# Optimization experiments

Hardware: AMD Instinct MI355X
Metric: run time of the kernel (lower is better)

The kernel has to match this reference:

```python
import jax
import jax.numpy as jnp
import numpy as np


def setup_inputs() -> dict:
    key = jax.random.key(0)
    k1, k2 = jax.random.split(key)
    B, C, H, W = 2, 256, 64, 128  # 1/8-res RAFT features of a 512x1024 image
    fmap1 = jax.random.normal(k1, (B, C, H, W), dtype=jnp.float32)
    fmap2 = jax.random.normal(k2, (B, C, H, W), dtype=jnp.float32)
    return {"fmap1": fmap1, "fmap2": fmap2, "k": 32}


def reference(fmap1, fmap2, k):
    B, C, H, W = fmap1.shape
    N = H * W
    f1 = fmap1.reshape(B, C, N)
    f2 = fmap2.reshape(B, C, N)

    # --- KNN (FAISS inner-product search), indices are non-differentiable ---
    scores = jnp.einsum('bcn,bcm->bnm', jax.lax.stop_gradient(f1),
                        jax.lax.stop_gradient(f2))  # [B, N1, N2]
    _, idx = jax.lax.top_k(scores, k)               # [B, N1, k]
    idx = jnp.transpose(idx, (0, 2, 1))             # [B, k, N1]

    # --- gather top-k target features: gathered[b,c,j,n] = f2[b,c,idx[b,j,n]] ---
    gathered = jax.vmap(lambda f, i: f[:, i])(f2, idx)  # [B, C, k, N1]

    # --- sparse correlation ---
    corr_sp = jnp.einsum('bcn,bckn->bkn', f1, gathered) / jnp.sqrt(jnp.float32(C))

    # --- coordinate grids (y-first), relative displacement ---
    ys, xs = jnp.meshgrid(jnp.arange(H, dtype=jnp.float32),
                          jnp.arange(W, dtype=jnp.float32), indexing='ij')
    coords = jnp.stack([ys.ravel(), xs.ravel()])          # [2, N], y first
    coords0 = jnp.broadcast_to(coords[None, :, None, :], (B, 2, k, N))
    coords1 = jnp.transpose(coords[:, idx], (1, 0, 2, 3))  # [B, 2, k, N]
    coords1 = coords1 - coords0                            # relative offsets

    batch_index = jnp.broadcast_to(
        jnp.arange(B, dtype=jnp.float32).reshape(B, 1, 1, 1), (B, 1, k, N))

    return corr_sp, coords0, coords1, batch_index
```

## Files before the change

kernel.cpp:

```cpp
#include <hip/hip_runtime.h>
#include <hip/hip_bf16.h>

#define B_  2
#define C_  256
#define H_  64
#define W_  128
#define N_  (H_ * W_)
#define K_  32
#define Q_  10
#define CK2 36
#define TN  32
#define TM  16
#define NHT 64
#define RR  32

typedef short  short8  __attribute__((ext_vector_type(8)));
typedef short  short4v __attribute__((ext_vector_type(4)));
typedef float  floatx4 __attribute__((ext_vector_type(4)));

__device__ __forceinline__ unsigned umin_(unsigned a, unsigned b) { return a < b ? a : b; }
__device__ __forceinline__ unsigned umax_(unsigned a, unsigned b) { return a > b ? a : b; }
__device__ __forceinline__ ushort f2bf(float v) {
    __hip_bfloat16 h = __float2bfloat16(v);
    ushort u; __builtin_memcpy(&u, &h, 2); return u;
}
__device__ __forceinline__ unsigned med3u(unsigned a, unsigned b, unsigned c) {
    unsigned d;
    asm("v_med3_u32 %0, %1, %2, %3" : "=v"(d) : "v"(a), "v"(b), "v"(c));
    return d;
}

__device__ __forceinline__ unsigned packkey(float v, int m) {
    const float vc = v > 0.0f ? v : 0.0f;
    unsigned b; __builtin_memcpy(&b, &vc, 4);
    return (b & 0xFFFFE000u) | (unsigned)m;
}

__device__ __forceinline__ void qinsert(unsigned (&q)[Q_], unsigned k) {
#pragma unroll
    for (int i = Q_ - 1; i > 0; --i)
        q[i] = med3u(q[i - 1], k, q[i]);
    q[0] = umax_(q[0], k);
}

#define CSWAP(a, b) { const unsigned _mx = umax_(a, b); \
                      const unsigned _mn = umin_(a, b); (a) = _mx; (b) = _mn; }

__device__ __forceinline__ void gl_lds16(const ushort* g, ushort* l) {
    __builtin_amdgcn_global_load_lds(
        (const __attribute__((address_space(1))) unsigned int*)(g),
        (__attribute__((address_space(3))) unsigned int*)(l),
        16, 0, 0);
}

__global__ void raft_prep_kernel(const float* __restrict__ f1,
                                 const float* __restrict__ f2,
                                 float* __restrict__ f1Tf,
                                 ushort* __restrict__ f2T,
                                 float* __restrict__ f2Tf) {
    __shared__ float tile[32][33];
    const int nt = blockIdx.x;
    const int ct = blockIdx.y;
    const int z  = blockIdx.z;
    const int b  = z >> 1;
    const float* __restrict__ src = (z & 1) ? f2 : f1;
    const int tid = threadIdx.x;

    {
        const int cl = tid >> 3;
        const int nx = tid & 7;
        const float4 v = *(const float4*)(
            src + ((size_t)b * C_ + (ct * 32 + cl)) * N_ + (nt * 32 + nx * 4));
        tile[cl][nx * 4 + 0] = v.x;
        tile[cl][nx * 4 + 1] = v.y;
        tile[cl][nx * 4 + 2] = v.z;
        tile[cl][nx * 4 + 3] = v.w;
    }
    __syncthreads();
    {
        const int nl = tid >> 3;
        const int c4 = (tid & 7) * 4;
        float4 v;
        v.x = tile[c4 + 0][nl];
        v.y = tile[c4 + 1][nl];
        v.z = tile[c4 + 2][nl];
        v.w = tile[c4 + 3][nl];
        const size_t o = ((size_t)b * N_ + (nt * 32 + nl)) * C_ + (ct * 32 + c4);
        if (z & 1) {
            *(float4*)(f2Tf + o) = v;
            short4v h;
            h[0] = (short)f2bf(v.x); h[1] = (short)f2bf(v.y);
            h[2] = (short)f2bf(v.z); h[3] = (short)f2bf(v.w);
            *(short4v*)(f2T + o) = h;
        } else {
            *(float4*)(f1Tf + o) = v;
        }
    }
}

__launch_bounds__(512, 4)
__global__ void raft_stage1_kernel(const float* __restrict__ f1Tf,
                                   const ushort* __restrict__ f2T,
                                   ushort* __restrict__ cand) {
    __shared__ __align__(16) ushort Bt[2][8][2048];

    const int bid0 = blockIdx.x;
    const int bid  = ((bid0 & 7) << 6) | (bid0 >> 3);
    const int b    = bid >> 8;
    const int nt0  = (bid & 255) * TN;
    const int tid  = threadIdx.x;
    const int w    = tid >> 6;
    const int lane = tid & 63;
    const int p    = lane & 15;
    const int q4   = lane >> 4;

    short8 af[2][8];
    #pragma unroll
    for (int ns = 0; ns < 2; ++ns) {
        const float* __restrict__ arow =
            f1Tf + ((size_t)b * N_ + nt0 + ns * 16 + p) * C_;
        #pragma unroll
        for (int ks = 0; ks < 8; ++ks) {
            const float4 x = *(const float4*)(arow + ks * 32 + q4 * 8);
            const float4 y = *(const float4*)(arow + ks * 32 + q4 * 8 + 4);
            short8 t;
            t[0] = (short)f2bf(x.x); t[1] = (short)f2bf(x.y);
            t[2] = (short)f2bf(x.z); t[3] = (short)f2bf(x.w);
            t[4] = (short)f2bf(y.x); t[5] = (short)f2bf(y.y);
            t[6] = (short)f2bf(y.z); t[7] = (short)f2bf(y.w);
            af[ns][ks] = t;
        }
    }

    unsigned q0[Q_], q1[Q_];
    #pragma unroll
    for (int i = 0; i < Q_; ++i) { q0[i] = 0u; q1[i] = 0u; }

    const ushort* __restrict__ f2Tb = f2T + (size_t)b * N_ * C_;
    const ushort* gsrc[4];
    #pragma unroll
    for (int i = 0; i < 4; ++i) {
        const int s  = w * 64 + i * 512 + lane;
        const int es = s >> 8;
        const int r  = (s >> 4) & 15;
        const int cc = (s & 15) ^ (r & 7);
        gsrc[i] = f2Tb + ((size_t)es * 1024 + r) * C_ + cc * 8;
    }
    const int sbase = (w * 64) * 8;

    #pragma unroll
    for (int i = 0; i < 4; ++i)
        gl_lds16(gsrc[i], &Bt[0][0][0] + sbase + i * 512 * 8);
    __syncthreads();

    floatx4 acc0, acc1;
    for (int mt = 0; mt < NHT; ++mt) {
        {
            const size_t off = (size_t)mt * TM * C_ + 128;
            #pragma unroll
            for (int i = 0; i < 4; ++i)
                gl_lds16(gsrc[i] + off, &Bt[1][0][0] + sbase + i * 512 * 8);
        }
        acc0 = (floatx4){0.f, 0.f, 0.f, 0.f};
        acc1 = (floatx4){0.f, 0.f, 0.f, 0.f};
        {
            const ushort* __restrict__ cur = &Bt[0][w][0];
            #pragma unroll
            for (int ks = 0; ks < 4; ++ks) {
                const int c = ks * 4 + q4;
                const short8 bm = *(const short8*)(&cur[(p * 16 + (c ^ (p & 7))) * 8]);
                acc0 = __builtin_amdgcn_mfma_f32_16x16x32_bf16(bm, af[0][ks], acc0, 0, 0, 0);
                acc1 = __builtin_amdgcn_mfma_f32_16x16x32_bf16(bm, af[1][ks], acc1, 0, 0, 0);
            }
        }
        __syncthreads();

        if (mt + 1 < NHT) {
            const size_t off = (size_t)(mt + 1) * TM * C_;
            #pragma unroll
            for (int i = 0; i < 4; ++i)
                gl_lds16(gsrc[i] + off, &Bt[0][0][0] + sbase + i * 512 * 8);
        }
        {
            const ushort* __restrict__ cur = &Bt[1][w][0];
            #pragma unroll
            for (int ks = 0; ks < 4; ++ks) {
                const int c = ks * 4 + q4;
                const short8 bm = *(const short8*)(&cur[(p * 16 + (c ^ (p & 7))) * 8]);
                acc0 = __builtin_amdgcn_mfma_f32_16x16x32_bf16(bm, af[0][4 + ks], acc0, 0, 0, 0);
                acc1 = __builtin_amdgcn_mfma_f32_16x16x32_bf16(bm, af[1][4 + ks], acc1, 0, 0, 0);
            }
        }

        const int mb = w * 1024 + mt * TM + q4 * 4;
        {
            unsigned k0 = packkey(acc0[0], mb + 0);
            unsigned k1 = packkey(acc0[1], mb + 1);
            unsigned k2 = packkey(acc0[2], mb + 2);
            unsigned k3 = packkey(acc0[3], mb + 3);
            CSWAP(k0, k1); CSWAP(k2, k3); CSWAP(k0, k2); CSWAP(k1, k3); CSWAP(k1, k2);
            qinsert(q0, k0);
            if (__any(k1 > q0[Q_ - 1])) {
                qinsert(q0, k1);
                if (__any(k2 > q0[Q_ - 1])) {
                    qinsert(q0, k2);
                    if (__any(k3 > q0[Q_ - 1])) qinsert(q0, k3);
                }
            }
        }
        {
            unsigned k0 = packkey(acc1[0], mb + 0);
            unsigned k1 = packkey(acc1[1], mb + 1);
            unsigned k2 = packkey(acc1[2], mb + 2);
            unsigned k3 = packkey(acc1[3], mb + 3);
            CSWAP(k0, k1); CSWAP(k2, k3); CSWAP(k0, k2); CSWAP(k1, k3); CSWAP(k1, k2);
            qinsert(q1, k0);
            if (__any(k1 > q1[Q_ - 1])) {
                qinsert(q1, k1);
                if (__any(k2 > q1[Q_ - 1])) {
                    qinsert(q1, k2);
                    if (__any(k3 > q1[Q_ - 1])) qinsert(q1, k3);
                }
            }
        }
        __syncthreads();
    }

    unsigned* __restrict__ smem = (unsigned*)&Bt[0][0][0];
    const int qi = w * 4 + q4;
    #pragma unroll
    for (int t = 0; t < Q_; ++t) {
        smem[(qi * Q_ + t) * 33 + p]      = q0[t];
        smem[(qi * Q_ + t) * 33 + 16 + p] = q1[t];
    }
    __syncthreads();

    unsigned* __restrict__ ms = smem + 10560;
    if (tid < 128) {
        const int r = tid >> 2, g = tid & 3;
        const int lb = g * 8;
        int i0 = 0, i1 = 0, i2 = 0, i3 = 0, i4 = 0, i5 = 0, i6 = 0, i7 = 0;
        for (int t = 0; t < CK2; ++t) {
            const unsigned a0 = (i0 < Q_) ? smem[((lb + 0) * Q_ + i0) * 33 + r] : 0u;
            const unsigned a1 = (i1 < Q_) ? smem[((lb + 1) * Q_ + i1) * 33 + r] : 0u;
            const unsigned a2 = (i2 < Q_) ? smem[((lb + 2) * Q_ + i2) * 33 + r] : 0u;
            const unsigned a3 = (i3 < Q_) ? smem[((lb + 3) * Q_ + i3) * 33 + r] : 0u;
            const unsigned a4 = (i4 < Q_) ? smem[((lb + 4) * Q_ + i4) * 33 + r] : 0u;
            const unsigned a5 = (i5 < Q_) ? smem[((lb + 5) * Q_ + i5) * 33 + r] : 0u;
            const unsigned a6 = (i6 < Q_) ? smem[((lb + 6) * Q_ + i6) * 33 + r] : 0u;
            const unsigned a7 = (i7 < Q_) ? smem[((lb + 7) * Q_ + i7) * 33 + r] : 0u;
            const unsigned mx = umax_(umax_(umax_(a0, a1), umax_(a2, a3)),
                                      umax_(umax_(a4, a5), umax_(a6, a7)));
            ms[(g * CK2 + t) * 33 + r] = mx;
            const bool e0 = (a0 == mx);
            const bool e1 = !e0 && (a1 == mx);
            const bool e2 = !e0 && !e1 && (a2 == mx);
            const bool e3 = !e0 && !e1 && !e2 && (a3 == mx);
            const bool e4 = !e0 && !e1 && !e2 && !e3 && (a4 == mx);
            const bool e5 = !e0 && !e1 && !e2 && !e3 && !e4 && (a5 == mx);
            const bool e6 = !e0 && !e1 && !e2 && !e3 && !e4 && !e5 && (a6 == mx);
            const bool e7 = !e0 && !e1 && !e2 && !e3 && !e4 && !e5 && !e6 && (a7 == mx);
            i0 += e0; i1 += e1; i2 += e2; i3 += e3;
            i4 += e4; i5 += e5; i6 += e6; i7 += e7;
        }
    }
    __syncthreads();

    if (tid < 32) {
        int i0 = 0, i1 = 0, i2 = 0, i3 = 0;
        ushort* __restrict__ myc = cand + ((size_t)(b * N_ + nt0 + tid)) * CK2;
        for (int t = 0; t < CK2; ++t) {
            const unsigned a0 = ms[(0 * CK2 + i0) * 33 + tid];
            const unsigned a1 = ms[(1 * CK2 + i1) * 33 + tid];
            const unsigned a2 = ms[(2 * CK2 + i2) * 33 + tid];
            const unsigned a3 = ms[(3 * CK2 + i3) * 33 + tid];
            const unsigned m01 = umax_(a0, a1), m23 = umax_(a2, a3);
            const unsigned mx  = umax_(m01, m23);
            myc[t] = (ushort)(mx & 0x1FFFu);
            i0 += (a0 == mx);
            i1 += (a0 != mx) & (a1 == mx);
            i2 += (a0 != mx) & (a1 != mx) & (a2 == mx);
            i3 += (a0 != mx) & (a1 != mx) & (a2 != mx) & (a3 == mx);
        }
    }
}

__launch_bounds__(576)
__global__ void raft_rerank_kernel(const float* __restrict__ f1Tf,
                                   const float* __restrict__ f2Tf,
                                   const ushort* __restrict__ cand,
                                   float* __restrict__ out) {
    __shared__ float  aS[RR][C_];
    __shared__ float  cs[RR][CK2];
    __shared__ ushort cmS[RR][CK2];
    const int bid0 = blockIdx.x;
    const int bid  = ((bid0 & 7) << 6) | (bid0 >> 3);
    const int row0 = bid * RR;
    const int tid  = threadIdx.x;
    const int bb   = row0 >> 13;

    for (int sidx = tid; sidx < RR * (C_ / 4); sidx += 576) {
        const int rr = sidx >> 6, s4 = sidx & 63;
        *(float4*)(&aS[rr][s4 * 4]) =
            *(const float4*)(f1Tf + ((size_t)(row0 + rr)) * C_ + s4 * 4);
    }
    const int rA = tid / CK2;
    const int cA = tid - rA * CK2;
    const int rB = rA + 16;
    cmS[rA][cA] = cand[(size_t)(row0 + rA) * CK2 + cA];
    cmS[rB][cA] = cand[(size_t)(row0 + rB) * CK2 + cA];
    __syncthreads();

    {
        const int mA = cmS[rA][cA];
        const int mB = cmS[rB][cA];
        const float* __restrict__ bRa = f2Tf + ((size_t)bb * N_ + mA) * C_;
        const float* __restrict__ bRb = f2Tf + ((size_t)bb * N_ + mB) * C_;
        float accA = 0.0f, accB = 0.0f;
        #pragma unroll 4
        for (int c4 = 0; c4 < C_; c4 += 4) {
            const float4 xA = *(const float4*)(bRa + c4);
            const float4 xB = *(const float4*)(bRb + c4);
            accA = fmaf(aS[rA][c4 + 0], xA.x, accA);
            accA = fmaf(aS[rA][c4 + 1], xA.y, accA);
            accA = fmaf(aS[rA][c4 + 2], xA.z, accA);
            accA = fmaf(aS[rA][c4 + 3], xA.w, accA);
            accB = fmaf(aS[rB][c4 + 0], xB.x, accB);
            accB = fmaf(aS[rB][c4 + 1], xB.y, accB);
            accB = fmaf(aS[rB][c4 + 2], xB.z, accB);
            accB = fmaf(aS[rB][c4 + 3], xB.w, accB);
        }
        cs[rA][cA] = accA;
        cs[rB][cA] = accB;
    }
    __syncthreads();

    #pragma unroll
    for (int pp = 0; pp < 2; ++pp) {
        const int r  = (pp == 0) ? rA : rB;
        const int c  = cA;
        const int rg = row0 + r;
        const int n  = rg & (N_ - 1);
        const int y0 = n >> 7, x0 = n & 127;
        {
            const float v = cs[r][c];
            const int m = cmS[r][c];
            int rank = 0;
            for (int j = 0; j < CK2; ++j) {
                const float vj = cs[r][j];
                rank += (vj > v) || ((vj == v) && (cmS[r][j] < m));
            }
            if (rank < K_) {
                const size_t posn = (size_t)rank * N_ + n;
                out[(size_t)bb * (K_ * N_) + posn] = v * 0.0625f;
                const size_t c1b = (size_t)1572864 + (size_t)bb * 2 * K_ * N_;
                out[c1b + posn]                     = (float)((m >> 7) - y0);
                out[c1b + (size_t)(K_ * N_) + posn] = (float)((m & 127) - x0);
            }
        }
        if (c < K_) {
            const size_t posn = (size_t)c * N_ + n;
            const size_t c0b = (size_t)524288 + (size_t)bb * 2 * K_ * N_;
            out[c0b + posn]                     = (float)y0;
            out[c0b + (size_t)(K_ * N_) + posn] = (float)x0;
            out[(size_t)2621440 + (size_t)bb * (K_ * N_) + posn] = (float)bb;
        }
    }
}

extern "C" void kernel_launch(void* const* d_in, const int* in_sizes, int n_in,
                              void* d_out, int out_size, void* d_ws, size_t ws_size,
                              hipStream_t stream) {
    const float* f1 = (const float*)d_in[0];
    const float* f2 = (const float*)d_in[1];

    float*  f1Tf = (float*)d_ws;
    float*  f2Tf = f1Tf + (size_t)B_ * N_ * C_;
    ushort* f2T  = (ushort*)(f2Tf + (size_t)B_ * N_ * C_);
    ushort* cand = f2T + (size_t)B_ * N_ * C_;

    raft_prep_kernel<<<dim3(N_ / 32, C_ / 32, B_ * 2), dim3(256), 0, stream>>>(
        f1, f2, f1Tf, f2T, f2Tf);

    raft_stage1_kernel<<<dim3(B_ * (N_ / TN)), dim3(512), 0, stream>>>(f1Tf, f2T, cand);

    raft_rerank_kernel<<<dim3(B_ * N_ / RR), dim3(576), 0, stream>>>(
        f1Tf, f2Tf, cand, (float*)d_out);
}
```

Measured before the change: 312.9 us.

## Give each wave a private 4-stage LDS ring to drop block barriers

The shared double-buffered B tile and its block-wide __syncthreads are replaced by a per-wave 4-slot ring in LDS. Each wave loads its own 64-column chunks with direct global-to-LDS copies and synchronises only through explicit vmcnt/lgkmcnt waits, keeping three chunks in flight. The aim is to remove inter-wave barrier stalls and deepen prefetch ahead of the MFMA and top-k work. It depends on hand-placed waitcnt and sched_barrier ordering, and removing the min-blocks launch bound may let register use grow and cut occupancy.

```diff
diff --git a/kernel.cpp b/kernel.cpp
--- a/kernel.cpp
+++ b/kernel.cpp
@@ -98,11 +98,11 @@
     }
 }
 
-__launch_bounds__(512, 4)
+__launch_bounds__(512)
 __global__ void raft_stage1_kernel(const float* __restrict__ f1Tf,
                                    const ushort* __restrict__ f2T,
                                    ushort* __restrict__ cand) {
-    __shared__ __align__(16) ushort Bt[2][8][2048];
+    __shared__ __align__(16) ushort Bt[8][4][1024];
 
     const int bid0 = blockIdx.x;
     const int bid  = ((bid0 & 7) << 6) | (bid0 >> 3);
@@ -136,61 +136,54 @@
     #pragma unroll
     for (int i = 0; i < Q_; ++i) { q0[i] = 0u; q1[i] = 0u; }
 
-    const ushort* __restrict__ f2Tb = f2T + (size_t)b * N_ * C_;
-    const ushort* gsrc[4];
-    #pragma unroll
-    for (int i = 0; i < 4; ++i) {
-        const int s  = w * 64 + i * 512 + lane;
-        const int es = s >> 8;
-        const int r  = (s >> 4) & 15;
-        const int cc = (s & 15) ^ (r & 7);
-        gsrc[i] = f2Tb + ((size_t)es * 1024 + r) * C_ + cc * 8;
-    }
-    const int sbase = (w * 64) * 8;
-
-    #pragma unroll
-    for (int i = 0; i < 4; ++i)
-        gl_lds16(gsrc[i], &Bt[0][0][0] + sbase + i * 512 * 8);
-    __syncthreads();
+    const int cc = (lane & 7) ^ ((lane >> 3) & 7);
+    const ushort* gq0 = f2T + (size_t)b * N_ * C_
+                      + ((size_t)w * 1024 + 0 * 8 + (lane >> 3)) * C_ + cc * 8;
+    const ushort* gq1 = gq0 + 8 * C_;
+
+    asm volatile("s_waitcnt vmcnt(0)" ::: "memory");
+    __builtin_amdgcn_sched_barrier(0);
+    gl_lds16(gq0,       &Bt[w][0][0]);  gl_lds16(gq1,       &Bt[w][0][512]);
+    gl_lds16(gq0 + 64,  &Bt[w][1][0]);  gl_lds16(gq1 + 64,  &Bt[w][1][512]);
+    gl_lds16(gq0 + 128, &Bt[w][2][0]);  gl_lds16(gq1 + 128, &Bt[w][2][512]);
+    __builtin_amdgcn_sched_barrier(0);
 
     floatx4 acc0, acc1;
+    #define WARF() { asm volatile("s_waitcnt lgkmcnt(0)" ::: "memory"); \
+                     __builtin_amdgcn_sched_barrier(0); }
+    #define WAITQ() { __builtin_amdgcn_sched_barrier(0); \
+                      asm volatile("s_waitcnt vmcnt(6)" ::: "memory"); \
+                      __builtin_amdgcn_sched_barrier(0); }
+    #define QCOMP(JB, KS0) { \
+        const short8 bmA = *(const short8*)( \
+            &Bt[w][JB][(p * 8 + ((q4) ^ (p & 7))) * 8]); \
+        acc0 = __builtin_amdgcn_mfma_f32_16x16x32_bf16(bmA, af[0][KS0], acc0, 0, 0, 0); \
+        acc1 = __builtin_amdgcn_mfma_f32_16x16x32_bf16(bmA, af[1][KS0], acc1, 0, 0, 0); \
+        const short8 bmB = *(const short8*)( \
+            &Bt[w][JB][(p * 8 + ((4 + q4) ^ (p & 7))) * 8]); \
+        acc0 = __builtin_amdgcn_mfma_f32_16x16x32_bf16(bmB, af[0][(KS0) + 1], acc0, 0, 0, 0); \
+        acc1 = __builtin_amdgcn_mfma_f32_16x16x32_bf16(bmB, af[1][(KS0) + 1], acc1, 0, 0, 0); }
+
     for (int mt = 0; mt < NHT; ++mt) {
-        {
-            const size_t off = (size_t)mt * TM * C_ + 128;
-            #pragma unroll
-            for (int i = 0; i < 4; ++i)
-                gl_lds16(gsrc[i] + off, &Bt[1][0][0] + sbase + i * 512 * 8);
-        }
         acc0 = (floatx4){0.f, 0.f, 0.f, 0.f};
         acc1 = (floatx4){0.f, 0.f, 0.f, 0.f};
-        {
-            const ushort* __restrict__ cur = &Bt[0][w][0];
-            #pragma unroll
-            for (int ks = 0; ks < 4; ++ks) {
-                const int c = ks * 4 + q4;
-                const short8 bm = *(const short8*)(&cur[(p * 16 + (c ^ (p & 7))) * 8]);
-                acc0 = __builtin_amdgcn_mfma_f32_16x16x32_bf16(bm, af[0][ks], acc0, 0, 0, 0);
-                acc1 = __builtin_amdgcn_mfma_f32_16x16x32_bf16(bm, af[1][ks], acc1, 0, 0, 0);
-            }
-        }
-        __syncthreads();
-
-        if (mt + 1 < NHT) {
-            const size_t off = (size_t)(mt + 1) * TM * C_;
-            #pragma unroll
-            for (int i = 0; i < 4; ++i)
-                gl_lds16(gsrc[i] + off, &Bt[0][0][0] + sbase + i * 512 * 8);
-        }
-        {
-            const ushort* __restrict__ cur = &Bt[1][w][0];
-            #pragma unroll
-            for (int ks = 0; ks < 4; ++ks) {
-                const int c = ks * 4 + q4;
-                const short8 bm = *(const short8*)(&cur[(p * 16 + (c ^ (p & 7))) * 8]);
-                acc0 = __builtin_amdgcn_mfma_f32_16x16x32_bf16(bm, af[0][4 + ks], acc0, 0, 0, 0);
-                acc1 = __builtin_amdgcn_mfma_f32_16x16x32_bf16(bm, af[1][4 + ks], acc1, 0, 0, 0);
-            }
-        }
+        WARF();
+        gl_lds16(gq0 + 192, &Bt[w][3][0]);  gl_lds16(gq1 + 192, &Bt[w][3][512]);
+        gq0 += 16 * C_;  gq1 += 16 * C_;
+        WAITQ();
+        QCOMP(0, 0);
+        WARF();
+        gl_lds16(gq0, &Bt[w][0][0]);        gl_lds16(gq1, &Bt[w][0][512]);
+        WAITQ();
+        QCOMP(1, 2);
+        WARF();
+        gl_lds16(gq0 + 64, &Bt[w][1][0]);   gl_lds16(gq1 + 64, &Bt[w][1][512]);
+        WAITQ();
+        QCOMP(2, 4);
+        WARF();
+        gl_lds16(gq0 + 128, &Bt[w][2][0]);  gl_lds16(gq1 + 128, &Bt[w][2][512]);
+        WAITQ();
+        QCOMP(3, 6);
 
         const int mb = w * 1024 + mt * TM + q4 * 4;
         {
@@ -223,8 +216,14 @@
                 }
             }
         }
-        __syncthreads();
-    }
+    }
+    #undef QCOMP
+    #undef WAITQ
+    #undef WARF
+
+    asm volatile("s_waitcnt vmcnt(0)" ::: "memory");
+    __builtin_amdgcn_sched_barrier(0);
+    __syncthreads();
 
     unsigned* __restrict__ smem = (unsigned*)&Bt[0][0][0];
     const int qi = w * 4 + q4;
```

Measured after the change: 322.9 us. +3.2%, slower.
